# Performance work log

Measured on AMD Instinct MI355X. Metric: run time of the kernel, lower is better.

The kernel has to match this reference:

```python
import jax, jax.numpy as jnp
import numpy as np

N_QUBITS = 12
N_LAYERS = 6
BATCH = 256
INPUT_DIM = 256
OUT_DIM = 64
PI = float(np.pi)


def _ry_mat(a):
    # a: scalar or (B,) real angle -> (...,2,2) complex64 RY matrix
    c, s = jnp.cos(a * 0.5), jnp.sin(a * 0.5)
    return jnp.stack([jnp.stack([c, -s], -1), jnp.stack([s, c], -1)], -2).astype(jnp.complex64)


def _rz_mat(a):
    # diag(e^{-i a/2}, e^{+i a/2})
    em = jnp.exp(-0.5j * a.astype(jnp.complex64))
    ep = jnp.exp(0.5j * a.astype(jnp.complex64))
    z = jnp.zeros_like(em)
    return jnp.stack([jnp.stack([em, z], -1), jnp.stack([z, ep], -1)], -2)


def _apply_1q(state, U, w):
    # shared (2,2) gate on wire w; state: (B, 2, ..., 2)
    s = jnp.moveaxis(state, w + 1, -1)
    s = jnp.einsum('ij,b...j->b...i', U, s)
    return jnp.moveaxis(s, -1, w + 1)


def _apply_1q_batched(state, U, w):
    # per-sample (B,2,2) gate on wire w
    s = jnp.moveaxis(state, w + 1, -1)
    s = jnp.einsum('bij,b...j->b...i', U, s)
    return jnp.moveaxis(s, -1, w + 1)


def _cnot(state, c, t):
    s0 = jnp.take(state, 0, axis=c + 1)
    s1 = jnp.take(state, 1, axis=c + 1)
    t_ax = t + 1 if t < c else t  # target axis index after removing control axis
    s1 = jnp.flip(s1, axis=t_ax)
    return jnp.stack([s0, s1], axis=c + 1)


def _cz(state, c, t):
    idx = [slice(None)] * (N_QUBITS + 1)
    idx[c + 1] = 1
    idx[t + 1] = 1
    return state.at[tuple(idx)].multiply(-1.0)


def _run_circuit(xq, q_weights):
    # xq: (B, n_qubits) in [-1,1]; forward passes xq*pi, circuit multiplies by pi again
    B = xq.shape[0]
    enc = xq * (PI * PI)
    state = jnp.zeros((B, 2 ** N_QUBITS), jnp.complex64).at[:, 0].set(1.0)
    state = state.reshape((B,) + (2,) * N_QUBITS)
    for i in range(N_QUBITS):
        state = _apply_1q_batched(state, _ry_mat(enc[:, i]), i)
    w = q_weights.reshape(N_LAYERS, N_QUBITS, 3)
    for layer in range(N_LAYERS):
        for i in range(N_QUBITS):
            # PennyLane order: RZ(w0) then RY(w1) then RZ(w2) -> U = RZ2 @ RY1 @ RZ0
            U = _rz_mat(w[layer, i, 2]) @ _ry_mat(w[layer, i, 1]) @ _rz_mat(w[layer, i, 0])
            state = _apply_1q(state, U, i)
        for i in range(N_QUBITS):
            state = _cnot(state, i, (i + 1) % N_QUBITS)
        if layer % 2 == 0 and layer < N_LAYERS - 1:
            for i in range(N_QUBITS):
                state = _apply_1q_batched(state, _ry_mat(enc[:, i] * 0.5), i)
        if layer % 2 == 1:
            for i in range(0, N_QUBITS - 2, 2):
                state = _cz(state, i, i + 2)
    # PauliZ expectation on wires 0,1,2
    p = (state.real ** 2 + state.imag ** 2).reshape(B, 2, 2, 2, -1).sum(-1)  # (B,2,2,2)
    z0 = (p[:, 0] - p[:, 1]).sum((-1, -2))
    z1 = (p[:, :, 0] - p[:, :, 1]).sum((-1, -2))
    z2 = (p[:, :, :, 0] - p[:, :, :, 1]).sum((-1, -2))
    return jnp.stack([z0, z1, z2], -1)  # (B, 3) float32


def _layernorm(h, g, b, eps=1e-5):
    mu = h.mean(-1, keepdims=True)
    var = ((h - mu) ** 2).mean(-1, keepdims=True)
    return (h - mu) * jax.lax.rsqrt(var + eps) * g + b


def _forward(x, W1, b1, g_ln, b_ln, W2, b2, W3, b3, q_weights, W4, b4, W5, b5):
    gelu = lambda t: jax.nn.gelu(t, approximate=False)
    h = gelu(x @ W1.T + b1)
    h = _layernorm(h, g_ln, b_ln)
    h = gelu(h @ W2.T + b2)
    xq = jnp.tanh(h @ W3.T + b3)  # (B, n_qubits)
    q = _run_circuit(xq, q_weights)  # (B, 3)
    return gelu(q @ W4.T + b4) @ W5.T + b5  # (B, OUT_DIM)


def setup_inputs() -> dict:
    key = jax.random.key(0)
    ks = jax.random.split(key, 8)
    rn = lambda k, shape, s=0.05: (jax.random.normal(k, shape) * s).astype(jnp.float32)
    return {
        'x': jax.random.normal(ks[0], (BATCH, INPUT_DIM), jnp.float32),
        'W1': rn(ks[1], (128, INPUT_DIM)), 'b1': jnp.zeros(128, jnp.float32),
        'g_ln': jnp.ones(128, jnp.float32), 'b_ln': jnp.zeros(128, jnp.float32),
        'W2': rn(ks[2], (64, 128)), 'b2': jnp.zeros(64, jnp.float32),
        'W3': rn(ks[3], (N_QUBITS, 64)), 'b3': jnp.zeros(N_QUBITS, jnp.float32),
        'q_weights': (jax.random.normal(ks[4], (N_LAYERS * N_QUBITS * 3,)) * 0.1).astype(jnp.float32),
        'W4': rn(ks[5], (32, 3)), 'b4': jnp.zeros(32, jnp.float32),
        'W5': rn(ks[6], (OUT_DIM, 32)), 'b5': jnp.zeros(OUT_DIM, jnp.float32),
    }


def reference(x, W1, b1, g_ln, b_ln, W2, b2, W3, b3, q_weights, W4, b4, W5, b5):
    return _forward(x, W1, b1, g_ln, b_ln, W2, b2, W3, b3, q_weights, W4, b4, W5, b5)
```

## Files before the change

kernel.cpp:

```cpp
#include <hip/hip_runtime.h>
#include <math.h>

#define NQ   12
#define NL   6
#define DIM  4096
#define BATCH 256
#define NT   512
#define PI2  9.869604401089358f

__device__ __forceinline__ float geluf(float x) {
    return 0.5f * x * (1.0f + erff(x * 0.70710678118654752f));
}

__device__ __forceinline__ int slotf(int j) { return j + (j >> 4); }

__device__ __forceinline__ float2 cmul(float2 a, float2 b) {
    return make_float2(fmaf(a.x, b.x, -a.y * b.y), fmaf(a.x, b.y, a.y * b.x));
}
__device__ __forceinline__ float2 cadd(float2 a, float2 b) {
    return make_float2(a.x + b.x, a.y + b.y);
}
__device__ __forceinline__ float2 cscale(float2 a, float s) {
    return make_float2(a.x * s, a.y * s);
}

__global__ __launch_bounds__(NT)
void qpu_kernel(const float* __restrict__ x,   const float* __restrict__ W1, const float* __restrict__ b1,
                const float* __restrict__ g_ln, const float* __restrict__ b_ln,
                const float* __restrict__ W2,  const float* __restrict__ b2,
                const float* __restrict__ W3,  const float* __restrict__ b3,
                const float* __restrict__ qw,  const float* __restrict__ W4, const float* __restrict__ b4,
                const float* __restrict__ W5,  const float* __restrict__ b5,
                float* __restrict__ out)
{
    __shared__ float2 st[2][DIM + DIM / 16];
    __shared__ float2 Um[NL * NQ * 4];
    __shared__ float  xs[256];
    __shared__ float  h1n[128];
    __shared__ float  h2s[64];
    __shared__ float  xqs[NQ];
    __shared__ float  musd[2];
    __shared__ float  qv[3];
    __shared__ float  h4s[32];
    __shared__ float  zred[8][3];

    const int t = threadIdx.x;
    const int b = blockIdx.x;

    if (t < 256) xs[t] = x[b * 256 + t];
    __syncthreads();

    if (t < 128) {
        const float4* w = (const float4*)(W1 + t * 256);
        float a0 = 0.f, a1 = 0.f, a2 = 0.f, a3 = 0.f;
        #pragma unroll 8
        for (int k = 0; k < 64; k++) {
            float4 wv = w[k];
            const float* xp = &xs[4 * k];
            a0 = fmaf(wv.x, xp[0], a0);
            a1 = fmaf(wv.y, xp[1], a1);
            a2 = fmaf(wv.z, xp[2], a2);
            a3 = fmaf(wv.w, xp[3], a3);
        }
        h1n[t] = geluf((a0 + a1) + (a2 + a3) + b1[t]);
    }
    __syncthreads();

    if (t < 64) {
        float v0 = h1n[t], v1 = h1n[t + 64];
        float s1 = v0 + v1;
        float s2 = fmaf(v0, v0, v1 * v1);
        #pragma unroll
        for (int off = 32; off > 0; off >>= 1) {
            s1 += __shfl_down(s1, off);
            s2 += __shfl_down(s2, off);
        }
        if (t == 0) {
            float mu  = s1 * (1.f / 128.f);
            float var = s2 * (1.f / 128.f) - mu * mu;
            musd[0] = mu;
            musd[1] = rsqrtf(var + 1e-5f);
        }
    }
    __syncthreads();
    if (t < 128) {
        h1n[t] = (h1n[t] - musd[0]) * musd[1] * g_ln[t] + b_ln[t];
    }
    __syncthreads();

    if (t < 64) {
        const float4* w = (const float4*)(W2 + t * 128);
        float a0 = 0.f, a1 = 0.f, a2 = 0.f, a3 = 0.f;
        #pragma unroll 8
        for (int k = 0; k < 32; k++) {
            float4 wv = w[k];
            const float* hp = &h1n[4 * k];
            a0 = fmaf(wv.x, hp[0], a0);
            a1 = fmaf(wv.y, hp[1], a1);
            a2 = fmaf(wv.z, hp[2], a2);
            a3 = fmaf(wv.w, hp[3], a3);
        }
        h2s[t] = geluf((a0 + a1) + (a2 + a3) + b2[t]);
    }
    __syncthreads();

    if (t < NQ) {
        const float4* w = (const float4*)(W3 + t * 64);
        float a0 = 0.f, a1 = 0.f, a2 = 0.f, a3 = 0.f;
        #pragma unroll
        for (int k = 0; k < 16; k++) {
            float4 wv = w[k];
            const float* hp = &h2s[4 * k];
            a0 = fmaf(wv.x, hp[0], a0);
            a1 = fmaf(wv.y, hp[1], a1);
            a2 = fmaf(wv.z, hp[2], a2);
            a3 = fmaf(wv.w, hp[3], a3);
        }
        xqs[t] = tanhf((a0 + a1) + (a2 + a3) + b3[t]);
    }
    __syncthreads();

    if (t < NL * NQ) {
        const int l = t / NQ;
        const int i = t % NQ;
        float a  = qw[t * 3 + 0];
        float bb = qw[t * 3 + 1];
        float c  = qw[t * 3 + 2];
        float sb, cb;   sincosf(0.5f * bb, &sb, &cb);
        float apc = 0.5f * (a + c), amc = 0.5f * (a - c);
        float sapc, capc; sincosf(apc, &sapc, &capc);
        float samc, camc; sincosf(amc, &samc, &camc);
        float2 u00 = make_float2( cb * capc, -cb * sapc);
        float2 u01 = make_float2(-sb * camc, -sb * samc);
        float2 u10 = make_float2( sb * camc, -sb * samc);
        float2 u11 = make_float2( cb * capc,  cb * sapc);

        float theta = 0.f;
        bool merge = false;
        if (l == 0)      { theta = xqs[i] * PI2;        merge = true; }
        else if (l & 1)  { theta = xqs[i] * PI2 * 0.5f; merge = true; }
        if (merge) {
            float sy, cy; sincosf(0.5f * theta, &sy, &cy);
            float2 m00 = cadd(cscale(u00,  cy), cscale(u01, sy));
            float2 m01 = cadd(cscale(u00, -sy), cscale(u01, cy));
            float2 m10 = cadd(cscale(u10,  cy), cscale(u11, sy));
            float2 m11 = cadd(cscale(u10, -sy), cscale(u11, cy));
            u00 = m00; u01 = m01; u10 = m10; u11 = m11;
        }
        Um[t * 4 + 0] = u00;
        Um[t * 4 + 1] = u01;
        Um[t * 4 + 2] = u10;
        Um[t * 4 + 3] = u11;
    }
    __syncthreads();

    float2 a[8];
    float z0 = 0.f, z1 = 0.f, z2 = 0.f;

    for (int l = 0; l < NL; l++) {
        const float2* UL  = &Um[l * NQ * 4];
        float2*       dst = st[l & 1];
        const float2* srcb = st[(l & 1) ^ 1];

        #pragma unroll
        for (int c = 0; c < 4; c++) {
            const int P    = 9 - 3 * c;
            const int low  = t & ((1 << P) - 1);
            const int base = ((t >> P) << (P + 3)) | low;

            if (c == 0) {
                if (l == 0) {
                    #pragma unroll
                    for (int m = 0; m < 8; m++) a[m] = make_float2(0.f, 0.f);
                    if (t == 0) a[0] = make_float2(1.f, 0.f);
                } else {
                    const bool czl = (l == 2) || (l == 4);
                    #pragma unroll
                    for (int m = 0; m < 8; m++) {
                        const int j = base | (m << 9);
                        const int src = ((j ^ (j >> 1)) & 0x3FF)
                                      | ((((j >> 10) ^ (j >> 11) ^ j) & 1) << 10)
                                      | ((((j >> 11) ^ j) & 1) << 11);
                        float2 v = srcb[slotf(src)];
                        if (czl) {
                            if (__popc(j & (j << 2) & 0xAA8) & 1) { v.x = -v.x; v.y = -v.y; }
                        }
                        a[m] = v;
                    }
                }
            } else {
                #pragma unroll
                for (int m = 0; m < 8; m++) a[m] = dst[slotf(base | (m << P))];
            }

            float2 uu[12];
            #pragma unroll
            for (int e = 0; e < 12; e++) uu[e] = UL[(3 * c) * 4 + e];
            #pragma unroll
            for (int k = 0; k < 3; k++) {
                const float2 u0 = uu[k * 4 + 0];
                const float2 u1 = uu[k * 4 + 1];
                const float2 u2 = uu[k * 4 + 2];
                const float2 u3 = uu[k * 4 + 3];
                const int bit = 4 >> k;
                #pragma unroll
                for (int m = 0; m < 8; m++) {
                    if (m & bit) continue;
                    float2 x0 = a[m], x1 = a[m | bit];
                    a[m]       = cadd(cmul(u0, x0), cmul(u1, x1));
                    a[m | bit] = cadd(cmul(u2, x0), cmul(u3, x1));
                }
            }

            if (!(l == NL - 1 && c == 3)) {
                #pragma unroll
                for (int m = 0; m < 8; m++) dst[slotf(base | (m << P))] = a[m];
                __syncthreads();
            }
        }
    }

    {
        float sp = 0.f, so = 0.f;
        #pragma unroll
        for (int m = 0; m < 8; m++) {
            float p = fmaf(a[m].x, a[m].x, a[m].y * a[m].y);
            if (__popc(m) & 1) so += p; else sp += p;
        }
        const float stot = sp + so;
        z0 = (__popc(t & 0xFF)  & 1) ? (so - sp) : (sp - so);
        z1 = (__popc(t & 0x180) & 1) ? -stot : stot;
        z2 = (__popc(t & 0x1C0) & 1) ? -stot : stot;
    }
    #pragma unroll
    for (int off = 32; off > 0; off >>= 1) {
        z0 += __shfl_down(z0, off);
        z1 += __shfl_down(z1, off);
        z2 += __shfl_down(z2, off);
    }
    if ((t & 63) == 0) {
        zred[t >> 6][0] = z0;
        zred[t >> 6][1] = z1;
        zred[t >> 6][2] = z2;
    }
    __syncthreads();
    if (t == 0) {
        float q0 = 0.f, q1 = 0.f, q2 = 0.f;
        #pragma unroll
        for (int w = 0; w < 8; w++) {
            q0 += zred[w][0]; q1 += zred[w][1]; q2 += zred[w][2];
        }
        qv[0] = q0; qv[1] = q1; qv[2] = q2;
    }
    __syncthreads();

    if (t < 32) {
        float h = b4[t];
        h = fmaf(qv[0], W4[t * 3 + 0], h);
        h = fmaf(qv[1], W4[t * 3 + 1], h);
        h = fmaf(qv[2], W4[t * 3 + 2], h);
        h4s[t] = geluf(h);
    }
    __syncthreads();
    if (t < 64) {
        float acc = b5[t];
        #pragma unroll
        for (int h = 0; h < 32; h++) acc = fmaf(h4s[h], W5[t * 32 + h], acc);
        out[b * 64 + t] = acc;
    }
}

extern "C" void kernel_launch(void* const* d_in, const int* in_sizes, int n_in,
                              void* d_out, int out_size, void* d_ws, size_t ws_size,
                              hipStream_t stream) {
    (void)in_sizes; (void)n_in; (void)d_ws; (void)ws_size; (void)out_size;
    const float* x    = (const float*)d_in[0];
    const float* W1   = (const float*)d_in[1];
    const float* b1   = (const float*)d_in[2];
    const float* g_ln = (const float*)d_in[3];
    const float* b_ln = (const float*)d_in[4];
    const float* W2   = (const float*)d_in[5];
    const float* b2   = (const float*)d_in[6];
    const float* W3   = (const float*)d_in[7];
    const float* b3   = (const float*)d_in[8];
    const float* qw   = (const float*)d_in[9];
    const float* W4   = (const float*)d_in[10];
    const float* b4   = (const float*)d_in[11];
    const float* W5   = (const float*)d_in[12];
    const float* b5   = (const float*)d_in[13];
    float* out = (float*)d_out;

    qpu_kernel<<<BATCH, NT, 0, stream>>>(x, W1, b1, g_ln, b_ln, W2, b2,
                                         W3, b3, qw, W4, b4, W5, b5, out);
}
```

Before: 113.5 us.

## Use closed-form product state for layer 0 and cross-lane exchanges for middle qubits

Layer 0 starts from |0…0⟩ with only single-qubit gates, so its output is computed directly as a tensor product of per-qubit amplitudes and the layer's shared-memory passes are skipped. Later layers keep three qubits in registers, handle six qubits with DPP/shuffle-xor exchanges between lanes, and use one shared-memory transpose to reach the remaining three. This cuts the LDS round-trips and barriers per layer from four to two, at the cost of many cross-lane operations and a heavier, harder-to-verify index mapping.

Result: faster. 110.3 us (-2.7%).

```diff
diff --git a/kernel.cpp b/kernel.cpp
--- a/kernel.cpp
+++ b/kernel.cpp
@@ -12,8 +12,6 @@
     return 0.5f * x * (1.0f + erff(x * 0.70710678118654752f));
 }
 
-__device__ __forceinline__ int slotf(int j) { return j + (j >> 4); }
-
 __device__ __forceinline__ float2 cmul(float2 a, float2 b) {
     return make_float2(fmaf(a.x, b.x, -a.y * b.y), fmaf(a.x, b.y, a.y * b.x));
 }
@@ -22,6 +20,34 @@
 }
 __device__ __forceinline__ float2 cscale(float2 a, float s) {
     return make_float2(a.x * s, a.y * s);
+}
+
+__device__ __forceinline__ int gmap(int j) {
+    return ((j ^ (j >> 1)) & 0x3FF)
+         | ((((j >> 10) ^ (j >> 11) ^ j) & 1) << 10)
+         | ((((j >> 11) ^ j) & 1) << 11);
+}
+
+template<int CTRL>
+__device__ __forceinline__ float2 dppx(float2 v) {
+    int x = __builtin_amdgcn_update_dpp(0, __float_as_int(v.x), CTRL, 0xF, 0xF, true);
+    int y = __builtin_amdgcn_update_dpp(0, __float_as_int(v.y), CTRL, 0xF, 0xF, true);
+    return make_float2(__int_as_float(x), __int_as_float(y));
+}
+
+__device__ __forceinline__ float2 shflx(float2 v, int mask) {
+    return make_float2(__shfl_xor(v.x, mask, 64), __shfl_xor(v.y, mask, 64));
+}
+
+__device__ __forceinline__ void reg_gate(float2* a, const float2* Ug, int bit) {
+    const float2 u00 = Ug[0], u01 = Ug[1], u10 = Ug[2], u11 = Ug[3];
+    #pragma unroll
+    for (int m = 0; m < 8; m++) {
+        if (m & bit) continue;
+        float2 x0 = a[m], x1 = a[m | bit];
+        a[m]       = cadd(cmul(u00, x0), cmul(u01, x1));
+        a[m | bit] = cadd(cmul(u10, x0), cmul(u11, x1));
+    }
 }
 
 __global__ __launch_bounds__(NT)
@@ -33,7 +59,8 @@
                 const float* __restrict__ W5,  const float* __restrict__ b5,
                 float* __restrict__ out)
 {
-    __shared__ float2 st[2][DIM + DIM / 16];
+    __shared__ float2 bufA[4352];
+    __shared__ float2 bufB[4352];
     __shared__ float2 Um[NL * NQ * 4];
     __shared__ float  xs[256];
     __shared__ float  h1n[128];
@@ -83,9 +110,7 @@
         }
     }
     __syncthreads();
-    if (t < 128) {
-        h1n[t] = (h1n[t] - musd[0]) * musd[1] * g_ln[t] + b_ln[t];
-    }
+    if (t < 128) h1n[t] = (h1n[t] - musd[0]) * musd[1] * g_ln[t] + b_ln[t];
     __syncthreads();
 
     if (t < 64) {
@@ -155,83 +180,105 @@
     __syncthreads();
 
     float2 a[8];
-    float z0 = 0.f, z1 = 0.f, z2 = 0.f;
-
-    for (int l = 0; l < NL; l++) {
-        const float2* UL  = &Um[l * NQ * 4];
-        float2*       dst = st[l & 1];
-        const float2* srcb = st[(l & 1) ^ 1];
-
-        #pragma unroll
-        for (int c = 0; c < 4; c++) {
-            const int P    = 9 - 3 * c;
-            const int low  = t & ((1 << P) - 1);
-            const int base = ((t >> P) << (P + 3)) | low;
-
-            if (c == 0) {
-                if (l == 0) {
-                    #pragma unroll
-                    for (int m = 0; m < 8; m++) a[m] = make_float2(0.f, 0.f);
-                    if (t == 0) a[0] = make_float2(1.f, 0.f);
-                } else {
-                    const bool czl = (l == 2) || (l == 4);
-                    #pragma unroll
-                    for (int m = 0; m < 8; m++) {
-                        const int j = base | (m << 9);
-                        const int src = ((j ^ (j >> 1)) & 0x3FF)
-                                      | ((((j >> 10) ^ (j >> 11) ^ j) & 1) << 10)
-                                      | ((((j >> 11) ^ j) & 1) << 11);
-                        float2 v = srcb[slotf(src)];
-                        if (czl) {
-                            if (__popc(j & (j << 2) & 0xAA8) & 1) { v.x = -v.x; v.y = -v.y; }
-                        }
-                        a[m] = v;
-                    }
-                }
-            } else {
-                #pragma unroll
-                for (int m = 0; m < 8; m++) a[m] = dst[slotf(base | (m << P))];
+    {
+        const float2* U0 = Um;
+        float2 P = ((t >> 0) & 1) ? U0[11 * 4 + 2] : U0[11 * 4 + 0];
+        #pragma unroll
+        for (int bb = 1; bb < 9; bb++) {
+            const float2* Uq = &U0[(11 - bb) * 4];
+            float2 fac = ((t >> bb) & 1) ? Uq[2] : Uq[0];
+            P = cmul(P, fac);
+        }
+        float2 b0 = cmul(P, U0[2 * 4 + 0]);
+        float2 b1 = cmul(P, U0[2 * 4 + 2]);
+        float2 a00 = cmul(b0, U0[1 * 4 + 0]);
+        float2 a01 = cmul(b1, U0[1 * 4 + 0]);
+        float2 a10 = cmul(b0, U0[1 * 4 + 2]);
+        float2 a11 = cmul(b1, U0[1 * 4 + 2]);
+        float2 f11 = U0[0 * 4 + 0], g11 = U0[0 * 4 + 2];
+        a[0] = cmul(a00, f11); a[1] = cmul(a01, f11);
+        a[2] = cmul(a10, f11); a[3] = cmul(a11, f11);
+        a[4] = cmul(a00, g11); a[5] = cmul(a01, g11);
+        a[6] = cmul(a10, g11); a[7] = cmul(a11, g11);
+    }
+
+    {
+        float2* wa = &bufA[t + (t >> 4)];
+        #pragma unroll
+        for (int m = 0; m < 8; m++) wa[m * 544] = a[m];
+        __syncthreads();
+        #pragma unroll
+        for (int m = 0; m < 8; m++) {
+            const int src = gmap(8 * t + m);
+            a[m] = bufA[src + (src >> 4)];
+        }
+    }
+
+    #pragma unroll 1
+    for (int l = 1; l < NL; l++) {
+        const float2* UL = &Um[l * NQ * 4];
+
+        reg_gate(a, &UL[11 * 4], 1);
+        reg_gate(a, &UL[10 * 4], 2);
+        reg_gate(a, &UL[ 9 * 4], 4);
+
+        #pragma unroll
+        for (int k = 0; k < 6; k++) {
+            const float2* Ug = &UL[(8 - k) * 4];
+            const float2 u00 = Ug[0], u01 = Ug[1], u10 = Ug[2], u11 = Ug[3];
+            const bool sel = (t >> k) & 1;
+            const float2 cA = sel ? u11 : u00;
+            const float2 cB = sel ? u10 : u01;
+            #pragma unroll
+            for (int m = 0; m < 8; m++) {
+                float2 v;
+                if      (k == 0) v = dppx<0xB1>(a[m]);
+                else if (k == 1) v = dppx<0x4E>(a[m]);
+                else             v = shflx(a[m], 1 << k);
+                a[m] = cadd(cmul(cA, a[m]), cmul(cB, v));
             }
-
-            float2 uu[12];
-            #pragma unroll
-            for (int e = 0; e < 12; e++) uu[e] = UL[(3 * c) * 4 + e];
-            #pragma unroll
-            for (int k = 0; k < 3; k++) {
-                const float2 u0 = uu[k * 4 + 0];
-                const float2 u1 = uu[k * 4 + 1];
-                const float2 u2 = uu[k * 4 + 2];
-                const float2 u3 = uu[k * 4 + 3];
-                const int bit = 4 >> k;
-                #pragma unroll
-                for (int m = 0; m < 8; m++) {
-                    if (m & bit) continue;
-                    float2 x0 = a[m], x1 = a[m | bit];
-                    a[m]       = cadd(cmul(u0, x0), cmul(u1, x1));
-                    a[m | bit] = cadd(cmul(u2, x0), cmul(u3, x1));
-                }
+        }
+
+        {
+            float2* wb = &bufB[8 * t + (t >> 1)];
+            #pragma unroll
+            for (int m = 0; m < 8; m++) wb[m] = a[m];
+            __syncthreads();
+            const float2* rb = &bufB[t + (t >> 4)];
+            #pragma unroll
+            for (int m = 0; m < 8; m++) a[m] = rb[m * 544];
+        }
+
+        reg_gate(a, &UL[2 * 4], 1);
+        reg_gate(a, &UL[1 * 4], 2);
+        reg_gate(a, &UL[0 * 4], 4);
+
+        if (l < NL - 1) {
+            float2* wa = &bufA[t + (t >> 4)];
+            #pragma unroll
+            for (int m = 0; m < 8; m++) wa[m * 544] = a[m];
+            __syncthreads();
+            const bool czl = (l == 1) || (l == 3);
+            #pragma unroll
+            for (int m = 0; m < 8; m++) {
+                const int j = 8 * t + m;
+                const int src = gmap(j);
+                float2 v = bufA[src + (src >> 4)];
+                if (czl && (__popc(j & (j << 2) & 0xAA8) & 1)) { v.x = -v.x; v.y = -v.y; }
+                a[m] = v;
             }
-
-            if (!(l == NL - 1 && c == 3)) {
-                #pragma unroll
-                for (int m = 0; m < 8; m++) dst[slotf(base | (m << P))] = a[m];
-                __syncthreads();
-            }
-        }
-    }
-
-    {
-        float sp = 0.f, so = 0.f;
-        #pragma unroll
-        for (int m = 0; m < 8; m++) {
-            float p = fmaf(a[m].x, a[m].x, a[m].y * a[m].y);
-            if (__popc(m) & 1) so += p; else sp += p;
-        }
-        const float stot = sp + so;
-        z0 = (__popc(t & 0xFF)  & 1) ? (so - sp) : (sp - so);
-        z1 = (__popc(t & 0x180) & 1) ? -stot : stot;
-        z2 = (__popc(t & 0x1C0) & 1) ? -stot : stot;
-    }
+        }
+    }
+
+    float p[8];
+    #pragma unroll
+    for (int m = 0; m < 8; m++) p[m] = fmaf(a[m].x, a[m].x, a[m].y * a[m].y);
+
+    float s03 = (p[0] - p[1] - p[2] + p[3]) + (p[4] - p[5] - p[6] + p[7]);
+    float z0 = (__popc(t) & 1) ? -s03 : s03;
+    float z1 = (p[0] + p[1]) - (p[2] + p[3]) - (p[4] + p[5]) + (p[6] + p[7]);
+    float z2 = (p[0] - p[1] - p[2] + p[3]) - (p[4] - p[5] - p[6] + p[7]);
+
     #pragma unroll
     for (int off = 32; off > 0; off >>= 1) {
         z0 += __shfl_down(z0, off);
```
